# Kernel optimization log

Measured on AMD Instinct MI355X. Metric: run time of the kernel, lower is better.

## Reference

```python
import jax, jax.numpy as jnp
import numpy as np

B, N, D, F_IN, F_OUT, MAX_DEG = 256, 512, 6, 128, 128, 6


def setup_inputs() -> dict:
    key = jax.random.key(0)
    k_atoms, k_deg, k_idx, k_w, k_b = jax.random.split(key, 5)
    atoms = jax.random.normal(k_atoms, (B, N, F_IN), dtype=jnp.float32)
    # structured edges: per-atom degree in [0, MAX_DEG-1], valid neighbor ids in
    # the first `deg` slots, -1 padding afterwards (NGFP convention)
    deg = jax.random.randint(k_deg, (B, N, 1), 0, MAX_DEG)
    nbr = jax.random.randint(k_idx, (B, N, D), 0, N)
    slot = jnp.arange(D)[None, None, :]
    edges = jnp.where(slot < deg, nbr, -1).astype(jnp.int64)
    W = jax.random.normal(k_w, (MAX_DEG, F_IN, F_OUT), dtype=jnp.float32) * (1.0 / np.sqrt(F_IN))
    b = jax.random.normal(k_b, (MAX_DEG, F_OUT), dtype=jnp.float32) * 0.01
    return {"atoms": atoms, "edges": edges, "W": W, "b": b}


def reference(atoms, edges, W, b):
    # lookup_neighbors with include_self=True: gather neighbor rows (-1 -> zero row)
    atoms_p = jnp.pad(atoms, ((0, 0), (1, 0), (0, 0)))          # [B, N+1, F]; row 0 is zeros
    gathered = jax.vmap(lambda a, e: a[e])(atoms_p, edges + 1)  # [B, N, D, F]
    summed = gathered.sum(axis=-2) + atoms                      # [B, N, F] (self included)
    degrees = (edges != -1).sum(axis=-1, keepdims=True)         # [B, N, 1]
    out = jnp.zeros(summed.shape[:-1] + (W.shape[-1],), dtype=summed.dtype)
    for d in range(MAX_DEG):
        h = jax.nn.relu(summed @ W[d] + b[d])                   # [B, N, F_OUT]
        out = out + h * (degrees == d).astype(summed.dtype)
    return out
```

## Files before the change

kernel.cpp:

```cpp
#include <hip/hip_runtime.h>


typedef short bf16x8 __attribute__((ext_vector_type(8)));
typedef float f32x4  __attribute__((ext_vector_type(4)));
typedef unsigned short ushort_t;
typedef unsigned int uint_t;

constexpr int Nn = 512;
constexpr int Ff = 128;

constexpr size_t WS_NEEDED = 196608;

__device__ inline ushort_t f2bf(float f) {
    uint_t u = __float_as_uint(f);
    return (ushort_t)((u + 0x7FFFu + ((u >> 16) & 1u)) >> 16);
}

__device__ inline bool detect_is64(const int* edges32) {
    int probe = edges32[2 * (threadIdx.x & 63) + 1];
    return __any(probe > 0) == 0;
}

__global__ __launch_bounds__(1024)
void k0_wt(const float* __restrict__ W, ushort_t* __restrict__ Wt) {
    int L = blockIdx.x * 1024 + threadIdx.x;
    int d = L >> 14, rem = L & 16383;
    int n = rem >> 7, k = rem & 127;
    Wt[L] = f2bf(W[(d << 14) + (k << 7) + n]);
}

__global__ __launch_bounds__(1024, 4)
void k_fused(const float* __restrict__ atoms,
             const int*   __restrict__ edges32,
             const ushort_t* __restrict__ Wt,
             const float* __restrict__ bias,
             float* __restrict__ out) {
    const int tid = threadIdx.x;
    const int mol = blockIdx.x;
    const bool is64 = detect_is64(edges32);

    __shared__ ushort_t summed[Nn * 136];
    __shared__ float4   abuf4[Nn * 2];
    __shared__ ushort_t rlist[Nn];
    __shared__ int hist[6], base_sh[8];

    const float4* gsrc = (const float4*)(atoms + (size_t)mol * (Nn * Ff));
    const int arow = tid >> 1, ac = tid & 1;
    float4 pf = gsrc[arow * 32 + ac];

    if (tid < 6) hist[tid] = 0;
    __syncthreads();
    int deg = 0, rk = 0;
    if (tid < Nn) {
        const size_t eb = (size_t)mol * (Nn * 6) + (size_t)tid * 6;
        #pragma unroll
        for (int j = 0; j < 6; j++) {
            int e = is64 ? edges32[(eb + j) * 2] : edges32[eb + j];
            deg += (e >= 0) ? 1 : 0;
        }
        if (deg > 5) deg = 5;
        rk = atomicAdd(&hist[deg], 1);
    }
    __syncthreads();
    if (tid == 0) {
        int a = 0;
        #pragma unroll
        for (int d = 0; d < 6; d++) { base_sh[d] = a; a += hist[d]; }
    }
    __syncthreads();
    if (tid < Nn) rlist[base_sh[deg] + rk] = (ushort_t)tid;
    abuf4[2 * arow + (ac ^ (arow & 1))] = pf;
    __syncthreads();

    const int pr = tid >> 1, h = tid & 1;
    const int R = rlist[pr];
    int er[6];
    {
        const size_t eb = (size_t)mol * (Nn * 6) + (size_t)R * 6;
        #pragma unroll
        for (int j = 0; j < 6; j++)
            er[j] = is64 ? edges32[(eb + j) * 2] : edges32[eb + j];
    }

    for (int s = 0; s < 16; s++) {
        if (s < 15) pf = gsrc[arow * 32 + (s + 1) * 2 + ac];
        float4 a = abuf4[2 * R + (h ^ (R & 1))];
        #pragma unroll
        for (int j = 0; j < 6; j++) {
            int e = er[j];
            if (e >= 0) {
                float4 v = abuf4[2 * e + (h ^ (e & 1))];
                a.x += v.x; a.y += v.y; a.z += v.z; a.w += v.w;
            }
        }
        uint2 o;
        o.x = (uint_t)f2bf(a.x) | ((uint_t)f2bf(a.y) << 16);
        o.y = (uint_t)f2bf(a.z) | ((uint_t)f2bf(a.w) << 16);
        *(uint2*)&summed[R * 136 + s * 8 + h * 4] = o;
        __syncthreads();
        if (s < 15) {
            abuf4[2 * arow + (ac ^ (arow & 1))] = pf;
            __syncthreads();
        }
    }

    const int lane = tid & 63, wid = tid >> 6;
    const int kq = lane >> 4, ml = lane & 15;

    int cnts[6], cbase[6], Tp[7];
    {
        int a = 0, b = 0;
        #pragma unroll
        for (int d = 0; d < 6; d++) {
            cnts[d] = hist[d];
            cbase[d] = b; b += cnts[d];
            Tp[d] = a; a += ((cnts[d] + 15) >> 4) * 4;
        }
        Tp[6] = a;
    }
    const int items = Tp[6];

    for (int it = wid; it < items; it += 16) {
        int d = 0;
        #pragma unroll
        for (int dd = 1; dd < 6; dd++) if (it >= Tp[dd]) d = dd;
        const int loc = it - Tp[d];
        const int ti = loc >> 2, ci = loc & 3;
        const int cn = cnts[d], cb = cbase[d];

        int lidx = ti * 16 + ml;
        int cl = (lidx < cn) ? lidx : cn - 1;
        int row = rlist[cb + cl];
        bf16x8 af[4];
        #pragma unroll
        for (int k0 = 0; k0 < 4; k0++)
            af[k0] = *(const bf16x8*)&summed[row * 136 + kq * 8 + k0 * 32];
        int orw[4];
        #pragma unroll
        for (int r = 0; r < 4; r++) {
            int li = ti * 16 + kq * 4 + r;
            orw[r] = (li < cn) ? (int)rlist[cb + li] : -1;
        }
        const ushort_t* wg = Wt + (size_t)d * 16384;
        #pragma unroll
        for (int n2 = 0; n2 < 2; n2++) {
            const int nt = ci * 2 + n2;
            bf16x8 bfr[4];
            #pragma unroll
            for (int k0 = 0; k0 < 4; k0++)
                bfr[k0] = *(const bf16x8*)&wg[(nt * 16 + ml) * 128 + k0 * 32 + kq * 8];
            f32x4 c = {0.f, 0.f, 0.f, 0.f};
            #pragma unroll
            for (int k0 = 0; k0 < 4; k0++)
                c = __builtin_amdgcn_mfma_f32_16x16x32_bf16(af[k0], bfr[k0], c, 0, 0, 0);
            const int col = nt * 16 + ml;
            const float bc = bias[d * Ff + col];
            #pragma unroll
            for (int r = 0; r < 4; r++) {
                if (orw[r] >= 0) {
                    float v = c[r] + bc;
                    out[((size_t)mol * Nn + orw[r]) * Ff + col] = v > 0.f ? v : 0.f;
                }
            }
        }
    }
}

__global__ __launch_bounds__(128, 2)
void graphconv_fallback(const float* __restrict__ atoms,
                        const int* __restrict__ edges_raw,
                        const float* __restrict__ W,
                        const float* __restrict__ bias,
                        float* __restrict__ out) {
    const int tid = threadIdx.x;
    const int d = blockIdx.x % 6;
    const int k = blockIdx.x / 6;
    const int a0 = k * 256;
    __shared__ int eds[256 * 6];
    __shared__ int list[256];
    __shared__ int cnt;
    __shared__ float sv[2][Ff];
    bool is64;
    { int v = edges_raw[2 * (tid & 63) + 1]; is64 = (__ballot(v > 0) == 0ull); }
    if (!is64) { for (int i = tid; i < 256 * 6; i += 128) eds[i] = edges_raw[a0 * 6 + i]; }
    else       { for (int i = tid; i < 256 * 6; i += 128) eds[i] = edges_raw[2 * (a0 * 6 + i)]; }
    if (tid == 0) cnt = 0;
    __syncthreads();
    for (int i = tid; i < 256; i += 128) {
        int deg = 0;
        #pragma unroll
        for (int j = 0; j < 6; j++) deg += (eds[i * 6 + j] != -1) ? 1 : 0;
        if (deg == d) { int p = atomicAdd(&cnt, 1); list[p] = i; }
    }
    float Wreg[Ff];
    { const float* Wd = W + (size_t)d * Ff * Ff;
      #pragma unroll
      for (int f = 0; f < Ff; f++) Wreg[f] = Wd[f * Ff + tid]; }
    const float breg = bias[d * Ff + tid];
    __syncthreads();
    const int n = cnt;
    const float* batch_atoms = atoms + (size_t)(a0 / Nn) * Nn * Ff;
    const int row0 = a0 % Nn;
    for (int ii = 0; ii < n; ii++) {
        const int i = list[ii];
        float s = batch_atoms[(row0 + i) * Ff + tid];
        #pragma unroll
        for (int j = 0; j < 6; j++) {
            int e = eds[i * 6 + j];
            if (e != -1) s += batch_atoms[e * Ff + tid];
        }
        float* buf = sv[ii & 1];
        buf[tid] = s;
        __syncthreads();
        float acc = breg;
        const float4* sv4 = (const float4*)buf;
        #pragma unroll
        for (int fc = 0; fc < Ff / 4; fc++) {
            float4 x = sv4[fc];
            acc = fmaf(x.x, Wreg[4 * fc + 0], acc);
            acc = fmaf(x.y, Wreg[4 * fc + 1], acc);
            acc = fmaf(x.z, Wreg[4 * fc + 2], acc);
            acc = fmaf(x.w, Wreg[4 * fc + 3], acc);
        }
        out[(size_t)(a0 + i) * Ff + tid] = fmaxf(acc, 0.0f);
    }
}

extern "C" void kernel_launch(void* const* d_in, const int* in_sizes, int n_in,
                              void* d_out, int out_size, void* d_ws, size_t ws_size,
                              hipStream_t stream) {
    const float* atoms = (const float*)d_in[0];
    const int*   edges = (const int*)d_in[1];
    const float* W     = (const float*)d_in[2];
    const float* bias  = (const float*)d_in[3];
    float*       outp  = (float*)d_out;

    if (ws_size >= WS_NEEDED) {
        ushort_t* Wt = (ushort_t*)d_ws;
        k0_wt<<<96, 1024, 0, stream>>>(W, Wt);
        k_fused<<<256, 1024, 0, stream>>>(atoms, edges, Wt, bias, outp);
    } else {
        graphconv_fallback<<<3072, 128, 0, stream>>>(atoms, edges, W, bias, outp);
    }
}
```

Baseline: 157.3 us.

## Split each molecule across four 256-thread blocks by row quarter

The fused kernel now launches four blocks per molecule, each owning 128 output rows, instead of one 1024-thread block per molecule. Each block still stages the full molecule's atom features in shared memory chunk by chunk, because neighbours can be any row. It then aggregates only its own rows and runs the degree-bucketed MFMA GEMM over them. This gives 1024 smaller blocks with a smaller shared footprint, meant to improve occupancy and load balance across CUs. The cost is that each molecule's atom data is loaded four times, and degree buckets are smaller, so more partial 16-row tiles waste work.

```diff
diff --git a/kernel.cpp b/kernel.cpp
--- a/kernel.cpp
+++ b/kernel.cpp
@@ -29,38 +29,47 @@
     Wt[L] = f2bf(W[(d << 14) + (k << 7) + n]);
 }
 
-__global__ __launch_bounds__(1024, 4)
+__global__ __launch_bounds__(256)
 void k_fused(const float* __restrict__ atoms,
              const int*   __restrict__ edges32,
              const ushort_t* __restrict__ Wt,
              const float* __restrict__ bias,
              float* __restrict__ out) {
     const int tid = threadIdx.x;
-    const int mol = blockIdx.x;
+    const int mol = blockIdx.x >> 2;
+    const int qr  = blockIdx.x & 3;
+    const int r0  = qr * 128;
     const bool is64 = detect_is64(edges32);
 
-    __shared__ ushort_t summed[Nn * 136];
+    __shared__ ushort_t summed[128 * 136];
     __shared__ float4   abuf4[Nn * 2];
-    __shared__ ushort_t rlist[Nn];
+    __shared__ ushort_t rlist[128];
     __shared__ int hist[6], base_sh[8];
 
     const float4* gsrc = (const float4*)(atoms + (size_t)mol * (Nn * Ff));
-    const int arow = tid >> 1, ac = tid & 1;
-    float4 pf = gsrc[arow * 32 + ac];
-
+    float4 pf[4];
+    #pragma unroll
+    for (int it = 0; it < 4; it++) {
+        int idx = tid + it * 256;
+        pf[it] = gsrc[(idx >> 1) * 32 + (idx & 1)];
+    }
+
+    const int pr = tid >> 1, h = tid & 1;
+    const int row_g = r0 + pr;
+    int er[6], deg = 0;
+    {
+        const size_t eb = (size_t)mol * (Nn * 6) + (size_t)row_g * 6;
+        #pragma unroll
+        for (int j = 0; j < 6; j++) {
+            er[j] = is64 ? edges32[(eb + j) * 2] : edges32[eb + j];
+            deg += (er[j] >= 0) ? 1 : 0;
+        }
+        if (deg > 5) deg = 5;
+    }
     if (tid < 6) hist[tid] = 0;
     __syncthreads();
-    int deg = 0, rk = 0;
-    if (tid < Nn) {
-        const size_t eb = (size_t)mol * (Nn * 6) + (size_t)tid * 6;
-        #pragma unroll
-        for (int j = 0; j < 6; j++) {
-            int e = is64 ? edges32[(eb + j) * 2] : edges32[eb + j];
-            deg += (e >= 0) ? 1 : 0;
-        }
-        if (deg > 5) deg = 5;
-        rk = atomicAdd(&hist[deg], 1);
-    }
+    int rk = 0;
+    if (h == 0) rk = atomicAdd(&hist[deg], 1);
     __syncthreads();
     if (tid == 0) {
         int a = 0;
@@ -68,23 +77,23 @@
         for (int d = 0; d < 6; d++) { base_sh[d] = a; a += hist[d]; }
     }
     __syncthreads();
-    if (tid < Nn) rlist[base_sh[deg] + rk] = (ushort_t)tid;
-    abuf4[2 * arow + (ac ^ (arow & 1))] = pf;
-    __syncthreads();
-
-    const int pr = tid >> 1, h = tid & 1;
-    const int R = rlist[pr];
-    int er[6];
-    {
-        const size_t eb = (size_t)mol * (Nn * 6) + (size_t)R * 6;
-        #pragma unroll
-        for (int j = 0; j < 6; j++)
-            er[j] = is64 ? edges32[(eb + j) * 2] : edges32[eb + j];
-    }
+    if (h == 0) rlist[base_sh[deg] + rk] = (ushort_t)pr;
+    #pragma unroll
+    for (int it = 0; it < 4; it++) {
+        int idx = tid + it * 256, r = idx >> 1, c = idx & 1;
+        abuf4[2 * r + (c ^ (r & 1))] = pf[it];
+    }
+    __syncthreads();
 
     for (int s = 0; s < 16; s++) {
-        if (s < 15) pf = gsrc[arow * 32 + (s + 1) * 2 + ac];
-        float4 a = abuf4[2 * R + (h ^ (R & 1))];
+        if (s < 15) {
+            #pragma unroll
+            for (int it = 0; it < 4; it++) {
+                int idx = tid + it * 256;
+                pf[it] = gsrc[(idx >> 1) * 32 + (s + 1) * 2 + (idx & 1)];
+            }
+        }
+        float4 a = abuf4[2 * row_g + (h ^ (row_g & 1))];
         #pragma unroll
         for (int j = 0; j < 6; j++) {
             int e = er[j];
@@ -96,10 +105,14 @@
         uint2 o;
         o.x = (uint_t)f2bf(a.x) | ((uint_t)f2bf(a.y) << 16);
         o.y = (uint_t)f2bf(a.z) | ((uint_t)f2bf(a.w) << 16);
-        *(uint2*)&summed[R * 136 + s * 8 + h * 4] = o;
+        *(uint2*)&summed[pr * 136 + s * 8 + h * 4] = o;
         __syncthreads();
         if (s < 15) {
-            abuf4[2 * arow + (ac ^ (arow & 1))] = pf;
+            #pragma unroll
+            for (int it = 0; it < 4; it++) {
+                int idx = tid + it * 256, r = idx >> 1, c = idx & 1;
+                abuf4[2 * r + (c ^ (r & 1))] = pf[it];
+            }
             __syncthreads();
         }
     }
@@ -120,7 +133,7 @@
     }
     const int items = Tp[6];
 
-    for (int it = wid; it < items; it += 16) {
+    for (int it = wid; it < items; it += 4) {
         int d = 0;
         #pragma unroll
         for (int dd = 1; dd < 6; dd++) if (it >= Tp[dd]) d = dd;
@@ -159,7 +172,7 @@
             for (int r = 0; r < 4; r++) {
                 if (orw[r] >= 0) {
                     float v = c[r] + bc;
-                    out[((size_t)mol * Nn + orw[r]) * Ff + col] = v > 0.f ? v : 0.f;
+                    out[((size_t)mol * Nn + r0 + orw[r]) * Ff + col] = v > 0.f ? v : 0.f;
                 }
             }
         }
@@ -238,7 +251,7 @@
     if (ws_size >= WS_NEEDED) {
         ushort_t* Wt = (ushort_t*)d_ws;
         k0_wt<<<96, 1024, 0, stream>>>(W, Wt);
-        k_fused<<<256, 1024, 0, stream>>>(atoms, edges, Wt, bias, outp);
+        k_fused<<<1024, 256, 0, stream>>>(atoms, edges, Wt, bias, outp);
     } else {
         graphconv_fallback<<<3072, 128, 0, stream>>>(atoms, edges, W, bias, outp);
     }
```

Result: slower. 335.4 us (+113.3%).

## Deepen atom prefetch to four stages and use LDS-only barriers in gather loop

Applied to the files above, without the earlier changes.

Turns the single-register global prefetch of atom slices into a 4-deep register ring, so global loads for later slices are issued several steps ahead of use. Replaces __syncthreads with an inline-asm barrier that waits only on LDS counters, so outstanding global prefetches are not drained at each barrier. Also loads the 64-bit edge indices of each row with vector uint4 reads and fully unrolls the 16-step loop. This costs extra registers in a kernel launched at 1024 threads, and it relies on the hand-written waitcnt being correct.

```diff
diff --git a/kernel.cpp b/kernel.cpp
--- a/kernel.cpp
+++ b/kernel.cpp
@@ -10,6 +10,8 @@
 constexpr int Ff = 128;
 
 constexpr size_t WS_NEEDED = 196608;
+
+#define BAR_LDS() asm volatile("s_waitcnt lgkmcnt(0)\ns_barrier" ::: "memory")
 
 __device__ inline ushort_t f2bf(float f) {
     uint_t u = __float_as_uint(f);
@@ -46,7 +48,9 @@
 
     const float4* gsrc = (const float4*)(atoms + (size_t)mol * (Nn * Ff));
     const int arow = tid >> 1, ac = tid & 1;
-    float4 pf = gsrc[arow * 32 + ac];
+    float4 pf[4];
+    #pragma unroll
+    for (int k = 0; k < 4; k++) pf[k] = gsrc[arow * 32 + k * 2 + ac];
 
     if (tid < 6) hist[tid] = 0;
     __syncthreads();
@@ -69,21 +73,27 @@
     }
     __syncthreads();
     if (tid < Nn) rlist[base_sh[deg] + rk] = (ushort_t)tid;
-    abuf4[2 * arow + (ac ^ (arow & 1))] = pf;
-    __syncthreads();
+    abuf4[2 * arow + (ac ^ (arow & 1))] = pf[0];
+    pf[0] = gsrc[arow * 32 + 4 * 2 + ac];
+    BAR_LDS();
 
     const int pr = tid >> 1, h = tid & 1;
     const int R = rlist[pr];
     int er[6];
-    {
-        const size_t eb = (size_t)mol * (Nn * 6) + (size_t)R * 6;
-        #pragma unroll
-        for (int j = 0; j < 6; j++)
-            er[j] = is64 ? edges32[(eb + j) * 2] : edges32[eb + j];
-    }
-
+    if (is64) {
+        const uint4* ep = (const uint4*)(edges32 + ((size_t)mol * (Nn * 6) + (size_t)R * 6) * 2);
+        uint4 q0 = ep[0], q1 = ep[1], q2 = ep[2];
+        er[0] = (int)q0.x; er[1] = (int)q0.z;
+        er[2] = (int)q1.x; er[3] = (int)q1.z;
+        er[4] = (int)q2.x; er[5] = (int)q2.z;
+    } else {
+        const int* ep = edges32 + (size_t)mol * (Nn * 6) + (size_t)R * 6;
+        #pragma unroll
+        for (int j = 0; j < 6; j++) er[j] = ep[j];
+    }
+
+    #pragma unroll
     for (int s = 0; s < 16; s++) {
-        if (s < 15) pf = gsrc[arow * 32 + (s + 1) * 2 + ac];
         float4 a = abuf4[2 * R + (h ^ (R & 1))];
         #pragma unroll
         for (int j = 0; j < 6; j++) {
@@ -97,12 +107,15 @@
         o.x = (uint_t)f2bf(a.x) | ((uint_t)f2bf(a.y) << 16);
         o.y = (uint_t)f2bf(a.z) | ((uint_t)f2bf(a.w) << 16);
         *(uint2*)&summed[R * 136 + s * 8 + h * 4] = o;
-        __syncthreads();
         if (s < 15) {
-            abuf4[2 * arow + (ac ^ (arow & 1))] = pf;
-            __syncthreads();
-        }
-    }
+            BAR_LDS();
+            abuf4[2 * arow + (ac ^ (arow & 1))] = pf[(s + 1) & 3];
+            if (s + 5 < 16)
+                pf[(s + 1) & 3] = gsrc[arow * 32 + (s + 5) * 2 + ac];
+            BAR_LDS();
+        }
+    }
+    BAR_LDS();
 
     const int lane = tid & 63, wid = tid >> 6;
     const int kq = lane >> 4, ml = lane & 15;
```

After: 183.8 us. 16.9% more time.
